# Performance work log

Measured on AMD Instinct MI355X. Metric: run time of the kernel, lower is better.

## Reference

```python
import jax, jax.numpy as jnp
import numpy as np


def _rotated_kernels(kernel, n_or):
    """Nearest-neighbour rotated copies of the kernel.

    kernel: [C, kOr, kH, kW] -> returns [n_or, C, kOr, kH, kW] where slice t is the
    kernel sampled at R_{2*pi*t/n_or}(y', x') about the kernel center; rotated
    coordinates that fall outside the kernel grid contribute zero.
    """
    C, kOr, kH, kW = kernel.shape
    cy = (kH - 1) / 2.0
    cx = (kW - 1) / 2.0
    ang = 2.0 * jnp.pi * jnp.arange(n_or, dtype=jnp.float32) / n_or
    ca = jnp.cos(ang)[:, None, None]  # [n_or,1,1]
    sa = jnp.sin(ang)[:, None, None]
    yy = jnp.arange(kH, dtype=jnp.float32)[:, None] - cy  # [kH,1]
    xx = jnp.arange(kW, dtype=jnp.float32)[None, :] - cx  # [1,kW]
    # rotate grid points by angle theta
    ys = sa * xx + ca * yy  # [n_or,kH,kW]
    xs = ca * xx - sa * yy
    iy = jnp.round(ys + cy).astype(jnp.int32)
    ix = jnp.round(xs + cx).astype(jnp.int32)
    mask = ((iy >= 0) & (iy < kH) & (ix >= 0) & (ix < kW)).astype(kernel.dtype)
    iyc = jnp.clip(iy, 0, kH - 1)
    ixc = jnp.clip(ix, 0, kW - 1)
    rot = kernel[:, :, iyc, ixc]            # [C,kOr,n_or,kH,kW] (gather)
    rot = rot * mask[None, None]            # zero out-of-grid samples
    return jnp.transpose(rot, (2, 0, 1, 3, 4))  # [n_or,C,kOr,kH,kW]


def setup_inputs() -> dict:
    key = jax.random.key(0)
    k1, k2 = jax.random.split(key)
    B, C, Or, H, W = 8, 32, 8, 128, 128
    kOr, kH, kW = 8, 5, 5
    x = jax.random.normal(k1, (B, C, Or, H, W), dtype=jnp.float32)
    # module parameter: uniform(-1, 1) per reset_parameters()
    kernel = jax.random.uniform(k2, (C, kOr, kH, kW), minval=-1.0, maxval=1.0,
                                dtype=jnp.float32)
    return {"x": x, "kernel": kernel}


def reference(x, kernel):
    """SE(2) linear (depthwise) group convolution.

    out[b,c,t,y,x] = sum_{t',y',x'} x[b,c,(t+t')%Or, y+y', x+x']
                     * kernel[c, t', NN(R_{2pi t/Or}(y', x'))]
    with centered, zero-padded spatial offsets ('SAME').
    """
    B, C, Or, H, W = x.shape
    _, kOr, kH, kW = kernel.shape
    rotk = _rotated_kernels(kernel, Or)  # [Or,C,kOr,kH,kW]
    dn = ('NCHW', 'OIHW', 'NCHW')
    out = jnp.zeros((B, C * Or, H, W), dtype=x.dtype)
    for tp in range(kOr):  # small fixed orientation-offset loop
        xs = jnp.roll(x, -tp, axis=2).reshape(B, C * Or, H, W)  # circular wrap in Or
        k = jnp.transpose(rotk[:, :, tp], (1, 0, 2, 3)).reshape(C * Or, 1, kH, kW)
        out = out + jax.lax.conv_general_dilated(
            xs, k, window_strides=(1, 1), padding='SAME',
            feature_group_count=C * Or, dimension_numbers=dn)
    return out.reshape(B, C, Or, H, W)
```

## Files before the change

kernel.cpp:

```cpp
#include <hip/hip_runtime.h>


typedef short bf16x8 __attribute__((ext_vector_type(8)));
typedef float f32x4 __attribute__((ext_vector_type(4)));

#define EPIL_TS 1092
#define EPIL_RP 68

__device__ inline unsigned short f2bf(float f) {
    unsigned int u = __float_as_uint(f);
    u += 0x7fffu + ((u >> 16) & 1u);
    return (unsigned short)(u >> 16);
}
__device__ inline unsigned pk2(float a, float b) {
    return (unsigned)f2bf(a) | ((unsigned)f2bf(b) << 16);
}

__device__ __constant__ float CA8[8] = {1.0f, 0.70710678f, 0.0f, -0.70710678f,
                                        -1.0f, -0.70710678f, 0.0f, 0.70710678f};
__device__ __constant__ float SA8[8] = {0.0f, 0.70710678f, 1.0f, 0.70710678f,
                                        0.0f, -0.70710678f, -1.0f, -0.70710678f};

__device__ inline float rot_w(const float* __restrict__ kern, int c, int t,
                              int o, int dy, int dx) {
    float ca = CA8[t], sa = SA8[t];
    float xx = (float)dx - 2.0f, yy = (float)dy - 2.0f;
    int iy = (int)rintf(sa * xx + ca * yy + 2.0f);
    int ix = (int)rintf(ca * xx - sa * yy + 2.0f);
    if (iy >= 0 && iy < 5 && ix >= 0 && ix < 5) {
        int tp = (o - t) & 7;
        return kern[(c * 8 + tp) * 25 + iy * 5 + ix];
    }
    return 0.0f;
}

__global__ __launch_bounds__(256)
void build_w2(const float* __restrict__ kern, unsigned short* __restrict__ wtab) {
    int e = blockIdx.x * 256 + threadIdx.x;
    if (e >= 131072) return;
    int o   = e & 7;
    int tr  = (e >> 3) & 31;
    int n16 = (e >> 8) & 15;
    int c   = e >> 12;
    int t   = n16 & 7, dlt = n16 >> 3;
    float w = 0.0f;
    if (tr < 30) {
        int dyr = tr / 5, dx = tr - 5 * dyr;
        int dy  = dyr - dlt;
        if (dy >= 0 && dy < 5) w = rot_w(kern, c, t, o, dy, dx);
    }
    wtab[e] = f2bf(w);
}

template <bool TAB>
__global__ __launch_bounds__(256)
void se2_mfma(const float* __restrict__ x, const float* __restrict__ kern,
              const unsigned short* __restrict__ wtab, float* __restrict__ out) {
    __shared__ __align__(16) float ldsbuf[5440];
    unsigned short* stage = reinterpret_cast<unsigned short*>(ldsbuf);
    float* epil = ldsbuf;

    const int bid = (blockIdx.x & 7) * 512 + (blockIdx.x >> 3);
    const int xh2 = bid & 1;
    const int ys  = (bid >> 1) & 7;
    const int bc  = bid >> 4;
    const int c   = bc & 31;
    const int X0  = xh2 * 64, Y0 = ys * 16;
    const int tid = threadIdx.x;

    const int lane = tid & 63;
    const int wv   = tid >> 6;
    const int g    = lane >> 4;
    const int m16  = lane & 15;

    const float* xbase = x + (size_t)bc * 131072;

    auto loadch = [&](int e, float (&v)[8]) {
        int r = e / 68, col = e - r * 68;
        int gy = Y0 - 2 + r, gx = X0 - 2 + col;
        if (gy >= 0 && gy < 128 && gx >= 0 && gx < 128) {
            const float* src = xbase + gy * 128 + gx;
#pragma unroll
            for (int o = 0; o < 8; ++o) v[o] = src[o * 16384];
        } else {
#pragma unroll
            for (int o = 0; o < 8; ++o) v[o] = 0.0f;
        }
    };
    auto packch = [&](int e, const float (&v)[8]) {
        *reinterpret_cast<uint4*>(&stage[e * 8]) =
            make_uint4(pk2(v[0], v[1]), pk2(v[2], v[3]),
                       pk2(v[4], v[5]), pk2(v[6], v[7]));
    };

    float sA[8], sB[8];
    loadch(tid, sA);
    loadch(tid + 256, sB);

    bf16x8 wfrag[8];
    int    tapoff[8];
#pragma unroll
    for (int cc = 0; cc < 8; ++cc) {
        int tr  = cc * 4 + g;
        int trc = tr < 30 ? tr : 29;
        int dyr = trc / 5, dx = trc - 5 * dyr;
        tapoff[cc] = (dyr * 68 + dx) * 8;
        if constexpr (TAB)
            wfrag[cc] = *reinterpret_cast<const bf16x8*>(
                &wtab[((c * 16 + m16) * 32 + tr) * 8]);
    }

    if constexpr (!TAB) {
        unsigned short* ldsw = stage;
        for (int e = tid; e < 4096; e += 256) {
            int o = e & 7, tr = (e >> 3) & 31, n16 = e >> 8;
            int t = n16 & 7, dlt = n16 >> 3;
            float w = 0.0f;
            if (tr < 30) {
                int dyr = tr / 5, dx = tr - 5 * dyr;
                int dy  = dyr - dlt;
                if (dy >= 0 && dy < 5) w = rot_w(kern, c, t, o, dy, dx);
            }
            ldsw[e] = f2bf(w);
        }
        __syncthreads();
#pragma unroll
        for (int cc = 0; cc < 8; ++cc)
            wfrag[cc] = *reinterpret_cast<const bf16x8*>(
                &ldsw[(m16 * 32 + cc * 4 + g) * 8]);
        __syncthreads();
    }

    packch(tid, sA);
    packch(tid + 256, sB);
    loadch(tid + 512, sA);
    loadch(tid + 768, sB);
    packch(tid + 512, sA);
    packch(tid + 768, sB);
    loadch(tid + 1024, sA);
    if (tid < 80) loadch(tid + 1280, sB);
    packch(tid + 1024, sA);
    if (tid < 80) packch(tid + 1280, sB);
    __syncthreads();

    f32x4 acc[8];
#pragma unroll
    for (int s = 0; s < 8; ++s) {
        acc[s] = (f32x4){0.f, 0.f, 0.f, 0.f};
        const int yl = wv * 4 + (s >> 2) * 2;
        const int baseS = (yl * 68 + (s & 3) * 16 + m16) * 8;
#pragma unroll
        for (int cc = 0; cc < 8; ++cc) {
            bf16x8 xf = *reinterpret_cast<const bf16x8*>(&stage[baseS + tapoff[cc]]);
            acc[s] = __builtin_amdgcn_mfma_f32_16x16x32_bf16(xf, wfrag[cc], acc[s], 0, 0, 0);
        }
    }
    __syncthreads();

    const int t_o = m16 & 7, dlt = m16 >> 3;
    const int exq = tid & 15;
    const int ey  = tid >> 4;
    float* outb = out + (size_t)bc * 131072;

#pragma unroll
    for (int p = 0; p < 2; ++p) {
        if (p) __syncthreads();
        if ((t_o >> 2) == p) {
#pragma unroll
            for (int s = 0; s < 8; ++s) {
                int y  = wv * 4 + (s >> 2) * 2 + dlt;
                int xx = (s & 3) * 16 + g * 4;
                *reinterpret_cast<f32x4*>(
                    &epil[(t_o & 3) * EPIL_TS + y * EPIL_RP + xx]) = acc[s];
            }
        }
        __syncthreads();
#pragma unroll
        for (int j = 0; j < 4; ++j) {
            f32x4 v = *reinterpret_cast<const f32x4*>(
                &epil[j * EPIL_TS + ey * EPIL_RP + exq * 4]);
            *reinterpret_cast<f32x4*>(
                outb + (size_t)(p * 4 + j) * 16384 +
                (size_t)(Y0 + ey) * 128 + X0 + exq * 4) = v;
        }
    }
}

extern "C" void kernel_launch(void* const* d_in, const int* in_sizes, int n_in,
                              void* d_out, int out_size, void* d_ws, size_t ws_size,
                              hipStream_t stream) {
    const float* x    = (const float*)d_in[0];
    const float* kern = (const float*)d_in[1];
    float* out = (float*)d_out;
    dim3 block(256);
    if (ws_size >= 131072 * sizeof(unsigned short)) {
        unsigned short* wtab = (unsigned short*)d_ws;
        build_w2<<<dim3(512), block, 0, stream>>>(kern, wtab);
        se2_mfma<true><<<dim3(4096), block, 0, stream>>>(x, kern, wtab, out);
    } else {
        se2_mfma<false><<<dim3(4096), block, 0, stream>>>(x, kern, nullptr, out);
    }
}
```

Measured before the change: 57.66 us.

## Widen tile to full 128-column rows and use nontemporal output stores

Each block now covers a full 128-wide by 16-row tile instead of a 64-wide half, so there are half as many blocks, each doing twice the MFMA work with 16 accumulators per wave. This cuts the redundant halo loads in the x direction and the per-block fixed costs such as weight-fragment loads. The epilogue is reorganized for the wider tile and writes output with nontemporal stores. The price is roughly double the LDS per block and more accumulator registers, which can lower occupancy.

```diff
diff --git a/kernel.cpp b/kernel.cpp
--- a/kernel.cpp
+++ b/kernel.cpp
@@ -4,8 +4,8 @@
 typedef short bf16x8 __attribute__((ext_vector_type(8)));
 typedef float f32x4 __attribute__((ext_vector_type(4)));
 
-#define EPIL_TS 1092
-#define EPIL_RP 68
+#define EPIL_TS 2116
+#define EPIL_RP 132
 
 __device__ inline unsigned short f2bf(float f) {
     unsigned int u = __float_as_uint(f);
@@ -56,16 +56,15 @@
 __global__ __launch_bounds__(256)
 void se2_mfma(const float* __restrict__ x, const float* __restrict__ kern,
               const unsigned short* __restrict__ wtab, float* __restrict__ out) {
-    __shared__ __align__(16) float ldsbuf[5440];
+    __shared__ __align__(16) float ldsbuf[10560];
     unsigned short* stage = reinterpret_cast<unsigned short*>(ldsbuf);
     float* epil = ldsbuf;
 
-    const int bid = (blockIdx.x & 7) * 512 + (blockIdx.x >> 3);
-    const int xh2 = bid & 1;
-    const int ys  = (bid >> 1) & 7;
-    const int bc  = bid >> 4;
+    const int bid = (blockIdx.x & 7) * 256 + (blockIdx.x >> 3);
+    const int ys  = bid & 7;
+    const int bc  = bid >> 3;
     const int c   = bc & 31;
-    const int X0  = xh2 * 64, Y0 = ys * 16;
+    const int Y0  = ys * 16;
     const int tid = threadIdx.x;
 
     const int lane = tid & 63;
@@ -76,8 +75,8 @@
     const float* xbase = x + (size_t)bc * 131072;
 
     auto loadch = [&](int e, float (&v)[8]) {
-        int r = e / 68, col = e - r * 68;
-        int gy = Y0 - 2 + r, gx = X0 - 2 + col;
+        int r = e / 132, col = e - r * 132;
+        int gy = Y0 - 2 + r, gx = col - 2;
         if (gy >= 0 && gy < 128 && gx >= 0 && gx < 128) {
             const float* src = xbase + gy * 128 + gx;
 #pragma unroll
@@ -104,14 +103,14 @@
         int tr  = cc * 4 + g;
         int trc = tr < 30 ? tr : 29;
         int dyr = trc / 5, dx = trc - 5 * dyr;
-        tapoff[cc] = (dyr * 68 + dx) * 8;
+        tapoff[cc] = (dyr * 132 + dx) * 8;
         if constexpr (TAB)
             wfrag[cc] = *reinterpret_cast<const bf16x8*>(
                 &wtab[((c * 16 + m16) * 32 + tr) * 8]);
     }
 
     if constexpr (!TAB) {
-        unsigned short* ldsw = stage;
+        unsigned short* ldsw = stage + 16384;
         for (int e = tid; e < 4096; e += 256) {
             int o = e & 7, tr = (e >> 3) & 31, n16 = e >> 8;
             int t = n16 & 7, dlt = n16 >> 3;
@@ -133,22 +132,22 @@
 
     packch(tid, sA);
     packch(tid + 256, sB);
-    loadch(tid + 512, sA);
-    loadch(tid + 768, sB);
-    packch(tid + 512, sA);
-    packch(tid + 768, sB);
-    loadch(tid + 1024, sA);
-    if (tid < 80) loadch(tid + 1280, sB);
-    packch(tid + 1024, sA);
-    if (tid < 80) packch(tid + 1280, sB);
+#pragma unroll 1
+    for (int kp = 1; kp < 5; ++kp) {
+        loadch(tid + kp * 512, sA);
+        loadch(tid + kp * 512 + 256, sB);
+        packch(tid + kp * 512, sA);
+        packch(tid + kp * 512 + 256, sB);
+    }
+    if (tid < 80) { loadch(2560 + tid, sA); packch(2560 + tid, sA); }
     __syncthreads();
 
-    f32x4 acc[8];
-#pragma unroll
-    for (int s = 0; s < 8; ++s) {
+    f32x4 acc[16];
+#pragma unroll
+    for (int s = 0; s < 16; ++s) {
         acc[s] = (f32x4){0.f, 0.f, 0.f, 0.f};
-        const int yl = wv * 4 + (s >> 2) * 2;
-        const int baseS = (yl * 68 + (s & 3) * 16 + m16) * 8;
+        const int yl = wv * 4 + (s >> 3) * 2;
+        const int baseS = (yl * 132 + (s & 7) * 16 + m16) * 8;
 #pragma unroll
         for (int cc = 0; cc < 8; ++cc) {
             bf16x8 xf = *reinterpret_cast<const bf16x8*>(&stage[baseS + tapoff[cc]]);
@@ -158,8 +157,6 @@
     __syncthreads();
 
     const int t_o = m16 & 7, dlt = m16 >> 3;
-    const int exq = tid & 15;
-    const int ey  = tid >> 4;
     float* outb = out + (size_t)bc * 131072;
 
 #pragma unroll
@@ -167,21 +164,25 @@
         if (p) __syncthreads();
         if ((t_o >> 2) == p) {
 #pragma unroll
-            for (int s = 0; s < 8; ++s) {
-                int y  = wv * 4 + (s >> 2) * 2 + dlt;
-                int xx = (s & 3) * 16 + g * 4;
+            for (int s = 0; s < 16; ++s) {
+                int y  = wv * 4 + (s >> 3) * 2 + dlt;
+                int xx = (s & 7) * 16 + g * 4;
                 *reinterpret_cast<f32x4*>(
                     &epil[(t_o & 3) * EPIL_TS + y * EPIL_RP + xx]) = acc[s];
             }
         }
         __syncthreads();
 #pragma unroll
-        for (int j = 0; j < 4; ++j) {
+        for (int j = 0; j < 8; ++j) {
+            int idx = j * 256 + tid;
+            int x4  = idx & 31;
+            int y   = (idx >> 5) & 15;
+            int t4  = idx >> 9;
             f32x4 v = *reinterpret_cast<const f32x4*>(
-                &epil[j * EPIL_TS + ey * EPIL_RP + exq * 4]);
-            *reinterpret_cast<f32x4*>(
-                outb + (size_t)(p * 4 + j) * 16384 +
-                (size_t)(Y0 + ey) * 128 + X0 + exq * 4) = v;
+                &epil[t4 * EPIL_TS + y * EPIL_RP + x4 * 4]);
+            __builtin_nontemporal_store(v, reinterpret_cast<f32x4*>(
+                outb + (size_t)(p * 4 + t4) * 16384 +
+                (size_t)(Y0 + y) * 128 + x4 * 4));
         }
     }
 }
@@ -196,8 +197,8 @@
     if (ws_size >= 131072 * sizeof(unsigned short)) {
         unsigned short* wtab = (unsigned short*)d_ws;
         build_w2<<<dim3(512), block, 0, stream>>>(kern, wtab);
-        se2_mfma<true><<<dim3(4096), block, 0, stream>>>(x, kern, wtab, out);
+        se2_mfma<true><<<dim3(2048), block, 0, stream>>>(x, kern, wtab, out);
     } else {
-        se2_mfma<false><<<dim3(4096), block, 0, stream>>>(x, kern, nullptr, out);
-    }
-}
+        se2_mfma<false><<<dim3(2048), block, 0, stream>>>(x, kern, nullptr, out);
+    }
+}
```

Measured after the change: 57.66 us. About the same (-0.0%).
